# Performance work log

Hardware: AMD Instinct MI355X
Metric: run time of the kernel (lower is better)

Reference implementation:

```python
import jax, jax.numpy as jnp
import numpy as np

N = 100000          # num_nodes
E = 1600000         # num_edges
D_IN = 128          # in_channels
H = 128             # hidden_channels
D_OUT = 128         # out_channels


def setup_inputs() -> dict:
    key = jax.random.key(0)
    ks = jax.random.split(key, 12)
    s = 1.0 / np.sqrt(H)
    inp = {
        "x": jax.random.normal(ks[0], (N, D_IN), dtype=jnp.float32),
        "edge_index": jax.random.randint(ks[1], (2, E), 0, N, dtype=jnp.int64),
        "edge_weight": jax.random.uniform(ks[2], (E,), dtype=jnp.float32),
        # edge_lin (SparseLinear): weight [num_nodes, hidden], bias [hidden]
        "W_edge": jax.random.uniform(ks[3], (N, H), jnp.float32, -1.0 / np.sqrt(N), 1.0 / np.sqrt(N)),
        "b_edge": jax.random.uniform(ks[4], (H,), jnp.float32, -1.0 / np.sqrt(N), 1.0 / np.sqrt(N)),
        # node_mlp: single Linear(in_channels, hidden)
        "W_node": jax.random.uniform(ks[5], (D_IN, H), jnp.float32, -1.0 / np.sqrt(D_IN), 1.0 / np.sqrt(D_IN)),
        "b_node": jax.random.uniform(ks[6], (H,), jnp.float32, -1.0 / np.sqrt(D_IN), 1.0 / np.sqrt(D_IN)),
        # cat_lin1 / cat_lin2: Linear(hidden, hidden)
        "W_cat1": jax.random.uniform(ks[7], (H, H), jnp.float32, -s, s),
        "b_cat1": jax.random.uniform(ks[8], (H,), jnp.float32, -s, s),
        "W_cat2": jax.random.uniform(ks[9], (H, H), jnp.float32, -s, s),
        "b_cat2": jax.random.uniform(ks[10], (H,), jnp.float32, -s, s),
        # final_mlp: single Linear(hidden, out_channels)
        "W_final": jax.random.uniform(ks[11], (H, D_OUT), jnp.float32, -s, s),
        "b_final": jax.random.uniform(jax.random.fold_in(key, 99), (D_OUT,), jnp.float32, -s, s),
    }
    return inp


def reference(x, edge_index, edge_weight, W_edge, b_edge, W_node, b_node,
              W_cat1, b_cat1, W_cat2, b_cat2, W_final, b_final):
    num_nodes = W_edge.shape[0]
    src, dst = edge_index[0], edge_index[1]
    # SparseLinear: out[i] = sum_{(j,i)} edge_weight * W_edge[j]  (SpMM A @ W)
    msg = edge_weight[:, None] * W_edge[src]                      # [E, H]
    out = jax.ops.segment_sum(msg, dst, num_segments=num_nodes)  # [N, H]
    out = out + b_edge
    # out = out + cat_lin1(out)
    out = out + out @ W_cat1 + b_cat1
    # x branch: node_mlp (single linear), then residual adds
    xh = x @ W_node + b_node                                      # [N, H]
    out = out + xh
    out = out + xh @ W_cat2 + b_cat2
    # final_mlp(relu(out)): single linear
    return jax.nn.relu(out) @ W_final + b_final
```

## Files before the change

### kernel.cpp

```cpp
#include <hip/hip_runtime.h>
#include <hip/hip_fp16.h>

#define NN 100000
#define NE 1600000
#define H  128
#define CAP 48

typedef short short8 __attribute__((ext_vector_type(8)));
typedef float f32x4 __attribute__((ext_vector_type(4)));

__device__ __forceinline__ unsigned short f2bf(float f) {
    unsigned int u = __float_as_uint(f);
    u = (u + 0x7fffu + ((u >> 16) & 1u)) >> 16;
    return (unsigned short)u;
}
__device__ __forceinline__ unsigned int packbf(float a, float b) {
    return (unsigned int)f2bf(a) | ((unsigned int)f2bf(b) << 16);
}
__device__ __forceinline__ unsigned char f2e5m2(float f) {
    unsigned short h = __half_as_ushort(__float2half_rn(f));
    h = (unsigned short)(h + 0x7F + ((h >> 8) & 1));
    return (unsigned char)(h >> 8);
}
__device__ __forceinline__ float e5m2lo(unsigned int u) {
    return __half2float(__ushort_as_half((unsigned short)((u << 8) & 0xFF00)));
}
__device__ __forceinline__ float e5m2hi(unsigned int u) {
    return __half2float(__ushort_as_half((unsigned short)(u & 0xFF00)));
}
__device__ __forceinline__ float entw(unsigned int e) {
    return __half2float(__ushort_as_half((unsigned short)((e & 0x7FFFu) << 1)));
}

__global__ void fill_kernel(const int* __restrict__ ei, const float* __restrict__ ew,
                            int* __restrict__ deg, unsigned int* __restrict__ bkt) {
    int e = blockIdx.x * 256 + threadIdx.x;
    if (e >= NE) return;
    int d = ei[NE + e];
    int pos = atomicAdd(&deg[d], 1);
    if (pos < CAP) {
        unsigned short h = __half_as_ushort(__float2half_rn(ew[e]));
        bkt[d * CAP + pos] = ((unsigned int)ei[e] << 15) | (h >> 1);
    }
}

__global__ __launch_bounds__(128) void prep_weights(const float* __restrict__ W_node,
                                                    const float* __restrict__ W_cat1,
                                                    const float* __restrict__ W_cat2,
                                                    const float* __restrict__ W_final,
                                                    const float* __restrict__ b_edge,
                                                    const float* __restrict__ b_node,
                                                    const float* __restrict__ b_cat1,
                                                    const float* __restrict__ b_cat2,
                                                    unsigned short* __restrict__ m2_t,
                                                    unsigned short* __restrict__ w3_t,
                                                    unsigned short* __restrict__ wf_t,
                                                    float* __restrict__ b4) {
    int t = threadIdx.x;
    int n = blockIdx.x;
    if (n < H) {
        __shared__ float c2col[H];
        c2col[t] = W_cat2[t * H + n];
        __syncthreads();
        float dot = 0.f;
        #pragma unroll 8
        for (int j = 0; j < H; ++j)
            dot += W_node[t * H + j] * c2col[j];
        float w3 = W_node[t * H + n] + dot;
        m2_t[n * H + t] = f2bf(W_cat1[t * H + n] + (t == n ? 1.f : 0.f));
        w3_t[n * H + t] = f2bf(w3);
        wf_t[n * H + t] = f2bf(W_final[t * H + n]);
    } else {
        __shared__ float be[H], bn[H];
        be[t] = b_edge[t];
        bn[t] = b_node[t];
        __syncthreads();
        float acc = be[t] + bn[t] + b_cat1[t] + b_cat2[t];
        for (int j = 0; j < H; ++j)
            acc += be[j] * W_cat1[j * H + t] + bn[j] * W_cat2[j * H + t];
        b4[t] = acc;
    }
}

__global__ __launch_bounds__(256) void gemm_we2(const float* __restrict__ W_edge,
                                                const unsigned short* __restrict__ m2_t,
                                                unsigned char* __restrict__ we8,
                                                int nrows) {
    const int TR = 32;
    __shared__ unsigned int Wsb[TR][64];
    int row0 = blockIdx.x * TR;
    int tid = threadIdx.x;

    for (int i = tid; i < TR * H / 4; i += 256) {
        int fi = i * 4;
        int rr = fi >> 7, cc = fi & 127;
        float4 v = {0.f, 0.f, 0.f, 0.f};
        if (row0 + rr < nrows)
            v = *reinterpret_cast<const float4*>(&W_edge[(long long)(row0 + rr) * H + cc]);
        int sw = (rr & 7) << 2;
        Wsb[rr][(cc >> 1) ^ sw]       = packbf(v.x, v.y);
        Wsb[rr][((cc >> 1) + 1) ^ sw] = packbf(v.z, v.w);
    }
    __syncthreads();

    int wv = tid >> 6, lane = tid & 63;
    int rt = wv & 1, ctb = (tid >> 7) * 4;
    int l15 = lane & 15, lhi = lane >> 4;
    int arow = rt * 16 + l15, asw = arow & 7;

    f32x4 zero4 = {0.f, 0.f, 0.f, 0.f};
    f32x4 acc[4];
    acc[0] = zero4; acc[1] = zero4; acc[2] = zero4; acc[3] = zero4;
    const short8* wrow = reinterpret_cast<const short8*>(&Wsb[arow][0]);

    #pragma unroll
    for (int kt = 0; kt < 4; ++kt) {
        short8 afrag = wrow[(kt * 4 + lhi) ^ asw];
        #pragma unroll
        for (int j = 0; j < 4; ++j) {
            short8 bfrag = *reinterpret_cast<const short8*>(
                &m2_t[((ctb + j) * 16 + l15) * H + kt * 32 + lhi * 8]);
            acc[j] = __builtin_amdgcn_mfma_f32_16x16x32_bf16(afrag, bfrag, acc[j], 0, 0, 0);
        }
    }

    #pragma unroll
    for (int j = 0; j < 4; ++j) {
        int colg = (ctb + j) * 16 + l15;
        #pragma unroll
        for (int r = 0; r < 4; ++r) {
            int row = row0 + rt * 16 + lhi * 4 + r;
            if (row < nrows)
                we8[(long long)row * H + colg] = f2e5m2(acc[j][r]);
        }
    }
}

#define EDGE2(jv, ax, ay)                                                   \
    {                                                                       \
        unsigned int e0 = bkt[jv];                                          \
        unsigned int e1 = bkt[jv + 1];                                      \
        unsigned int u0 = we8u[(e0 >> 15) * 64 + lane];                     \
        unsigned int u1 = we8u[(e1 >> 15) * 64 + lane];                     \
        float w0 = entw(e0), w1 = entw(e1);                                 \
        ax += w0 * e5m2lo(u0) + w1 * e5m2lo(u1);                            \
        ay += w0 * e5m2hi(u0) + w1 * e5m2hi(u1);                            \
    }

#define EDGE1(jv, ax, ay)                                                   \
    {                                                                       \
        unsigned int e = bkt[jv];                                           \
        unsigned int u = we8u[(e >> 15) * 64 + lane];                       \
        float w = entw(e);                                                  \
        ax += w * e5m2lo(u);                                                \
        ay += w * e5m2hi(u);                                                \
    }

__global__ __launch_bounds__(256) void gather_fused(const int* __restrict__ deg,
                                                    const unsigned int* __restrict__ bkt,
                                                    const unsigned short* __restrict__ we8u,
                                                    const float* __restrict__ x,
                                                    const unsigned short* __restrict__ w3_t,
                                                    const float* __restrict__ b4,
                                                    const unsigned short* __restrict__ wf_t,
                                                    const float* __restrict__ bf,
                                                    float* __restrict__ out,
                                                    int nrows) {
    const int TR = 32;
    __shared__ unsigned int Xsb[TR][64];
    __shared__ float Gs[TR][132];
    int row0 = blockIdx.x * TR;
    int tid = threadIdx.x;

    for (int i = tid; i < TR * H / 4; i += 256) {
        int fi = i * 4;
        int rr = fi >> 7, cc = fi & 127;
        float4 xv = *reinterpret_cast<const float4*>(&x[(long long)(row0 + rr) * H + cc]);
        int sw = (rr & 7) << 2;
        Xsb[rr][(cc >> 1) ^ sw]       = packbf(xv.x, xv.y);
        Xsb[rr][((cc >> 1) + 1) ^ sw] = packbf(xv.z, xv.w);
    }

    int wv = tid >> 6;
    int lane = tid & 63;
    #pragma unroll
    for (int rq = 0; rq < 2; ++rq) {
        int rrA = wv * 8 + rq * 4;
        int dA = row0 + rrA;
        float axA = 0.f, ayA = 0.f, axB = 0.f, ayB = 0.f;
        float axC = 0.f, ayC = 0.f, axD = 0.f, ayD = 0.f;

        int dgA = __builtin_amdgcn_readfirstlane(deg[dA]);
        int dgB = __builtin_amdgcn_readfirstlane(deg[dA + 1]);
        int dgC = __builtin_amdgcn_readfirstlane(deg[dA + 2]);
        int dgD = __builtin_amdgcn_readfirstlane(deg[dA + 3]);
        if (dgA > CAP) dgA = CAP;
        if (dgB > CAP) dgB = CAP;
        if (dgC > CAP) dgC = CAP;
        if (dgD > CAP) dgD = CAP;
        int jA = dA * CAP,      i1A = jA + dgA;
        int jB = (dA + 1) * CAP, i1B = jB + dgB;
        int jC = (dA + 2) * CAP, i1C = jC + dgC;
        int jD = (dA + 3) * CAP, i1D = jD + dgD;

        while (jA + 2 <= i1A && jB + 2 <= i1B && jC + 2 <= i1C && jD + 2 <= i1D) {
            unsigned int eA0 = bkt[jA];
            unsigned int eA1 = bkt[jA + 1];
            unsigned int eB0 = bkt[jB];
            unsigned int eB1 = bkt[jB + 1];
            unsigned int eC0 = bkt[jC];
            unsigned int eC1 = bkt[jC + 1];
            unsigned int eD0 = bkt[jD];
            unsigned int eD1 = bkt[jD + 1];
            unsigned int uA0 = we8u[(eA0 >> 15) * 64 + lane];
            unsigned int uA1 = we8u[(eA1 >> 15) * 64 + lane];
            unsigned int uB0 = we8u[(eB0 >> 15) * 64 + lane];
            unsigned int uB1 = we8u[(eB1 >> 15) * 64 + lane];
            unsigned int uC0 = we8u[(eC0 >> 15) * 64 + lane];
            unsigned int uC1 = we8u[(eC1 >> 15) * 64 + lane];
            unsigned int uD0 = we8u[(eD0 >> 15) * 64 + lane];
            unsigned int uD1 = we8u[(eD1 >> 15) * 64 + lane];
            float wA0 = entw(eA0), wA1 = entw(eA1);
            float wB0 = entw(eB0), wB1 = entw(eB1);
            float wC0 = entw(eC0), wC1 = entw(eC1);
            float wD0 = entw(eD0), wD1 = entw(eD1);
            axA += wA0 * e5m2lo(uA0) + wA1 * e5m2lo(uA1);
            ayA += wA0 * e5m2hi(uA0) + wA1 * e5m2hi(uA1);
            axB += wB0 * e5m2lo(uB0) + wB1 * e5m2lo(uB1);
            ayB += wB0 * e5m2hi(uB0) + wB1 * e5m2hi(uB1);
            axC += wC0 * e5m2lo(uC0) + wC1 * e5m2lo(uC1);
            ayC += wC0 * e5m2hi(uC0) + wC1 * e5m2hi(uC1);
            axD += wD0 * e5m2lo(uD0) + wD1 * e5m2lo(uD1);
            ayD += wD0 * e5m2hi(uD0) + wD1 * e5m2hi(uD1);
            jA += 2; jB += 2; jC += 2; jD += 2;
        }
        while (jA + 2 <= i1A && jB + 2 <= i1B) {
            EDGE2(jA, axA, ayA)
            EDGE2(jB, axB, ayB)
            jA += 2; jB += 2;
        }
        for (; jA + 2 <= i1A; jA += 2) EDGE2(jA, axA, ayA)
        if (jA < i1A) EDGE1(jA, axA, ayA)
        for (; jB + 2 <= i1B; jB += 2) EDGE2(jB, axB, ayB)
        if (jB < i1B) EDGE1(jB, axB, ayB)
        while (jC + 2 <= i1C && jD + 2 <= i1D) {
            EDGE2(jC, axC, ayC)
            EDGE2(jD, axD, ayD)
            jC += 2; jD += 2;
        }
        for (; jC + 2 <= i1C; jC += 2) EDGE2(jC, axC, ayC)
        if (jC < i1C) EDGE1(jC, axC, ayC)
        for (; jD + 2 <= i1D; jD += 2) EDGE2(jD, axD, ayD)
        if (jD < i1D) EDGE1(jD, axD, ayD)

        *reinterpret_cast<float2*>(&Gs[rrA][2 * lane])     = make_float2(axA, ayA);
        *reinterpret_cast<float2*>(&Gs[rrA + 1][2 * lane]) = make_float2(axB, ayB);
        *reinterpret_cast<float2*>(&Gs[rrA + 2][2 * lane]) = make_float2(axC, ayC);
        *reinterpret_cast<float2*>(&Gs[rrA + 3][2 * lane]) = make_float2(axD, ayD);
    }
    __syncthreads();

    int rt = wv & 1, ctb = (tid >> 7) * 4;
    int l15 = lane & 15, lhi = lane >> 4;
    int arow = rt * 16 + l15, asw = arow & 7;

    f32x4 acc[4];
    #pragma unroll
    for (int j = 0; j < 4; ++j) {
        int colg = (ctb + j) * 16 + l15;
        float bv = b4[colg];
        #pragma unroll
        for (int r = 0; r < 4; ++r)
            acc[j][r] = Gs[rt * 16 + lhi * 4 + r][colg] + bv;
    }
    __syncthreads();

    const short8* xsrow = reinterpret_cast<const short8*>(&Xsb[arow][0]);
    #pragma unroll
    for (int kt = 0; kt < 4; ++kt) {
        short8 afrag = xsrow[(kt * 4 + lhi) ^ asw];
        #pragma unroll
        for (int j = 0; j < 4; ++j) {
            short8 bfrag = *reinterpret_cast<const short8*>(
                &w3_t[((ctb + j) * 16 + l15) * H + kt * 32 + lhi * 8]);
            acc[j] = __builtin_amdgcn_mfma_f32_16x16x32_bf16(afrag, bfrag, acc[j], 0, 0, 0);
        }
    }

    unsigned short* t4s = reinterpret_cast<unsigned short*>(Gs);
    #pragma unroll
    for (int j = 0; j < 4; ++j) {
        int colg = (ctb + j) * 16 + l15;
        #pragma unroll
        for (int r = 0; r < 4; ++r) {
            int row = rt * 16 + lhi * 4 + r;
            float v = fmaxf(acc[j][r], 0.f);
            t4s[row * 128 + (colg ^ ((row & 7) << 3))] = f2bf(v);
        }
    }
    __syncthreads();

    f32x4 zero4 = {0.f, 0.f, 0.f, 0.f};
    f32x4 acc2[4];
    acc2[0] = zero4; acc2[1] = zero4; acc2[2] = zero4; acc2[3] = zero4;
    const short8* t4row = reinterpret_cast<const short8*>(t4s + arow * 128);

    #pragma unroll
    for (int kt = 0; kt < 4; ++kt) {
        short8 afrag = t4row[(kt * 4 + lhi) ^ asw];
        #pragma unroll
        for (int j = 0; j < 4; ++j) {
            short8 bfrag = *reinterpret_cast<const short8*>(
                &wf_t[((ctb + j) * 16 + l15) * H + kt * 32 + lhi * 8]);
            acc2[j] = __builtin_amdgcn_mfma_f32_16x16x32_bf16(afrag, bfrag, acc2[j], 0, 0, 0);
        }
    }

    #pragma unroll
    for (int j = 0; j < 4; ++j) {
        int colg = (ctb + j) * 16 + l15;
        float bv = bf[colg];
        #pragma unroll
        for (int r = 0; r < 4; ++r) {
            int row = row0 + rt * 16 + lhi * 4 + r;
            out[(long long)row * H + colg] = acc2[j][r] + bv;
        }
    }
}

extern "C" void kernel_launch(void* const* d_in, const int* in_sizes, int n_in,
                              void* d_out, int out_size, void* d_ws, size_t ws_size,
                              hipStream_t stream) {
    const float* x       = (const float*)d_in[0];
    const int*   ei      = (const int*)d_in[1];
    const float* ew      = (const float*)d_in[2];
    const float* W_edge  = (const float*)d_in[3];
    const float* b_edge  = (const float*)d_in[4];
    const float* W_node  = (const float*)d_in[5];
    const float* b_node  = (const float*)d_in[6];
    const float* W_cat1  = (const float*)d_in[7];
    const float* b_cat1  = (const float*)d_in[8];
    const float* W_cat2  = (const float*)d_in[9];
    const float* b_cat2  = (const float*)d_in[10];
    const float* W_final = (const float*)d_in[11];
    const float* b_final = (const float*)d_in[12];
    float* out = (float*)d_out;

    int* deg = (int*)d_ws;
    unsigned int* bkt = (unsigned int*)(deg + NN);
    unsigned char* we8 = (unsigned char*)(bkt + (size_t)NN * CAP);
    unsigned short* m2_t = (unsigned short*)(we8 + (size_t)NN * H);
    unsigned short* w3_t = m2_t + H * H;
    unsigned short* wf_t = w3_t + H * H;
    float* b4 = (float*)(wf_t + H * H);

    hipMemsetAsync(deg, 0, NN * sizeof(int), stream);
    fill_kernel<<<(NE + 255) / 256, 256, 0, stream>>>(ei, ew, deg, bkt);

    prep_weights<<<H + 1, H, 0, stream>>>(W_node, W_cat1, W_cat2, W_final,
                                          b_edge, b_node, b_cat1, b_cat2,
                                          m2_t, w3_t, wf_t, b4);
    gemm_we2<<<(NN + 31) / 32, 256, 0, stream>>>(W_edge, m2_t, we8, NN);

    gather_fused<<<(NN + 31) / 32, 256, 0, stream>>>(deg, bkt, (const unsigned short*)we8,
                                                     x, w3_t, b4, wf_t, b_final, out, NN);
}
```

Measured before the change: 305.7 us.

## Interleave eight destination rows per wave and fold degree zeroing into prep kernel

The gather loop now walks all eight of a wave's destination rows together, so each iteration issues sixteen independent bucket and W_edge row loads instead of eight, raising memory-level parallelism for the random gathers. The separate hipMemsetAsync of the degree array is replaced by extra blocks in prep_weights, removing one launch and moving prep_weights ahead of fill_kernel. The cost is more live registers in gather_fused, which may lower occupancy, and the eight-way loop exits as soon as the shortest of the eight rows runs out, leaving more work to the pairwise tail loops.

```diff
diff --git a/kernel.cpp b/kernel.cpp
--- a/kernel.cpp
+++ b/kernel.cpp
@@ -55,7 +55,8 @@
                                                     unsigned short* __restrict__ m2_t,
                                                     unsigned short* __restrict__ w3_t,
                                                     unsigned short* __restrict__ wf_t,
-                                                    float* __restrict__ b4) {
+                                                    float* __restrict__ b4,
+                                                    int* __restrict__ deg) {
     int t = threadIdx.x;
     int n = blockIdx.x;
     if (n < H) {
@@ -70,7 +71,7 @@
         m2_t[n * H + t] = f2bf(W_cat1[t * H + n] + (t == n ? 1.f : 0.f));
         w3_t[n * H + t] = f2bf(w3);
         wf_t[n * H + t] = f2bf(W_final[t * H + n]);
-    } else {
+    } else if (n == H) {
         __shared__ float be[H], bn[H];
         be[t] = b_edge[t];
         bn[t] = b_node[t];
@@ -79,6 +80,9 @@
         for (int j = 0; j < H; ++j)
             acc += be[j] * W_cat1[j * H + t] + bn[j] * W_cat2[j * H + t];
         b4[t] = acc;
+    } else {
+        int i = (n - H - 1) * 128 + t;
+        if (i < NN) deg[i] = 0;
     }
 }
 
@@ -154,6 +158,14 @@
         float w = entw(e);                                                  \
         ax += w * e5m2lo(u);                                                \
         ay += w * e5m2hi(u);                                                \
+    }
+
+#define STEP8(eN0, eN1, uN0, uN1, jv, ax, ay)                               \
+    {                                                                       \
+        float w0 = entw(eN0), w1 = entw(eN1);                               \
+        ax += w0 * e5m2lo(uN0) + w1 * e5m2lo(uN1);                          \
+        ay += w0 * e5m2hi(uN0) + w1 * e5m2hi(uN1);                          \
+        jv += 2;                                                            \
     }
 
 __global__ __launch_bounds__(256) void gather_fused(const int* __restrict__ deg,
@@ -183,35 +195,48 @@
 
     int wv = tid >> 6;
     int lane = tid & 63;
-    #pragma unroll
-    for (int rq = 0; rq < 2; ++rq) {
-        int rrA = wv * 8 + rq * 4;
-        int dA = row0 + rrA;
+    {
+        int base = row0 + wv * 8;
         float axA = 0.f, ayA = 0.f, axB = 0.f, ayB = 0.f;
         float axC = 0.f, ayC = 0.f, axD = 0.f, ayD = 0.f;
-
-        int dgA = __builtin_amdgcn_readfirstlane(deg[dA]);
-        int dgB = __builtin_amdgcn_readfirstlane(deg[dA + 1]);
-        int dgC = __builtin_amdgcn_readfirstlane(deg[dA + 2]);
-        int dgD = __builtin_amdgcn_readfirstlane(deg[dA + 3]);
+        float axE = 0.f, ayE = 0.f, axF = 0.f, ayF = 0.f;
+        float axG = 0.f, ayG = 0.f, axH = 0.f, ayH = 0.f;
+
+        int dgA = __builtin_amdgcn_readfirstlane(deg[base]);
+        int dgB = __builtin_amdgcn_readfirstlane(deg[base + 1]);
+        int dgC = __builtin_amdgcn_readfirstlane(deg[base + 2]);
+        int dgD = __builtin_amdgcn_readfirstlane(deg[base + 3]);
+        int dgE = __builtin_amdgcn_readfirstlane(deg[base + 4]);
+        int dgF = __builtin_amdgcn_readfirstlane(deg[base + 5]);
+        int dgG = __builtin_amdgcn_readfirstlane(deg[base + 6]);
+        int dgH = __builtin_amdgcn_readfirstlane(deg[base + 7]);
         if (dgA > CAP) dgA = CAP;
         if (dgB > CAP) dgB = CAP;
         if (dgC > CAP) dgC = CAP;
         if (dgD > CAP) dgD = CAP;
-        int jA = dA * CAP,      i1A = jA + dgA;
-        int jB = (dA + 1) * CAP, i1B = jB + dgB;
-        int jC = (dA + 2) * CAP, i1C = jC + dgC;
-        int jD = (dA + 3) * CAP, i1D = jD + dgD;
-
-        while (jA + 2 <= i1A && jB + 2 <= i1B && jC + 2 <= i1C && jD + 2 <= i1D) {
-            unsigned int eA0 = bkt[jA];
-            unsigned int eA1 = bkt[jA + 1];
-            unsigned int eB0 = bkt[jB];
-            unsigned int eB1 = bkt[jB + 1];
-            unsigned int eC0 = bkt[jC];
-            unsigned int eC1 = bkt[jC + 1];
-            unsigned int eD0 = bkt[jD];
-            unsigned int eD1 = bkt[jD + 1];
+        if (dgE > CAP) dgE = CAP;
+        if (dgF > CAP) dgF = CAP;
+        if (dgG > CAP) dgG = CAP;
+        if (dgH > CAP) dgH = CAP;
+        int jA = base * CAP,        i1A = jA + dgA;
+        int jB = (base + 1) * CAP,  i1B = jB + dgB;
+        int jC = (base + 2) * CAP,  i1C = jC + dgC;
+        int jD = (base + 3) * CAP,  i1D = jD + dgD;
+        int jE = (base + 4) * CAP,  i1E = jE + dgE;
+        int jF = (base + 5) * CAP,  i1F = jF + dgF;
+        int jG = (base + 6) * CAP,  i1G = jG + dgG;
+        int jH = (base + 7) * CAP,  i1H = jH + dgH;
+
+        while (jA + 2 <= i1A && jB + 2 <= i1B && jC + 2 <= i1C && jD + 2 <= i1D &&
+               jE + 2 <= i1E && jF + 2 <= i1F && jG + 2 <= i1G && jH + 2 <= i1H) {
+            unsigned int eA0 = bkt[jA], eA1 = bkt[jA + 1];
+            unsigned int eB0 = bkt[jB], eB1 = bkt[jB + 1];
+            unsigned int eC0 = bkt[jC], eC1 = bkt[jC + 1];
+            unsigned int eD0 = bkt[jD], eD1 = bkt[jD + 1];
+            unsigned int eE0 = bkt[jE], eE1 = bkt[jE + 1];
+            unsigned int eF0 = bkt[jF], eF1 = bkt[jF + 1];
+            unsigned int eG0 = bkt[jG], eG1 = bkt[jG + 1];
+            unsigned int eH0 = bkt[jH], eH1 = bkt[jH + 1];
             unsigned int uA0 = we8u[(eA0 >> 15) * 64 + lane];
             unsigned int uA1 = we8u[(eA1 >> 15) * 64 + lane];
             unsigned int uB0 = we8u[(eB0 >> 15) * 64 + lane];
@@ -220,43 +245,53 @@
             unsigned int uC1 = we8u[(eC1 >> 15) * 64 + lane];
             unsigned int uD0 = we8u[(eD0 >> 15) * 64 + lane];
             unsigned int uD1 = we8u[(eD1 >> 15) * 64 + lane];
-            float wA0 = entw(eA0), wA1 = entw(eA1);
-            float wB0 = entw(eB0), wB1 = entw(eB1);
-            float wC0 = entw(eC0), wC1 = entw(eC1);
-            float wD0 = entw(eD0), wD1 = entw(eD1);
-            axA += wA0 * e5m2lo(uA0) + wA1 * e5m2lo(uA1);
-            ayA += wA0 * e5m2hi(uA0) + wA1 * e5m2hi(uA1);
-            axB += wB0 * e5m2lo(uB0) + wB1 * e5m2lo(uB1);
-            ayB += wB0 * e5m2hi(uB0) + wB1 * e5m2hi(uB1);
-            axC += wC0 * e5m2lo(uC0) + wC1 * e5m2lo(uC1);
-            ayC += wC0 * e5m2hi(uC0) + wC1 * e5m2hi(uC1);
-            axD += wD0 * e5m2lo(uD0) + wD1 * e5m2lo(uD1);
-            ayD += wD0 * e5m2hi(uD0) + wD1 * e5m2hi(uD1);
-            jA += 2; jB += 2; jC += 2; jD += 2;
-        }
-        while (jA + 2 <= i1A && jB + 2 <= i1B) {
-            EDGE2(jA, axA, ayA)
-            EDGE2(jB, axB, ayB)
-            jA += 2; jB += 2;
-        }
+            unsigned int uE0 = we8u[(eE0 >> 15) * 64 + lane];
+            unsigned int uE1 = we8u[(eE1 >> 15) * 64 + lane];
+            unsigned int uF0 = we8u[(eF0 >> 15) * 64 + lane];
+            unsigned int uF1 = we8u[(eF1 >> 15) * 64 + lane];
+            unsigned int uG0 = we8u[(eG0 >> 15) * 64 + lane];
+            unsigned int uG1 = we8u[(eG1 >> 15) * 64 + lane];
+            unsigned int uH0 = we8u[(eH0 >> 15) * 64 + lane];
+            unsigned int uH1 = we8u[(eH1 >> 15) * 64 + lane];
+            STEP8(eA0, eA1, uA0, uA1, jA, axA, ayA)
+            STEP8(eB0, eB1, uB0, uB1, jB, axB, ayB)
+            STEP8(eC0, eC1, uC0, uC1, jC, axC, ayC)
+            STEP8(eD0, eD1, uD0, uD1, jD, axD, ayD)
+            STEP8(eE0, eE1, uE0, uE1, jE, axE, ayE)
+            STEP8(eF0, eF1, uF0, uF1, jF, axF, ayF)
+            STEP8(eG0, eG1, uG0, uG1, jG, axG, ayG)
+            STEP8(eH0, eH1, uH0, uH1, jH, axH, ayH)
+        }
+        while (jA + 2 <= i1A && jB + 2 <= i1B) { EDGE2(jA, axA, ayA) EDGE2(jB, axB, ayB) jA += 2; jB += 2; }
         for (; jA + 2 <= i1A; jA += 2) EDGE2(jA, axA, ayA)
         if (jA < i1A) EDGE1(jA, axA, ayA)
         for (; jB + 2 <= i1B; jB += 2) EDGE2(jB, axB, ayB)
         if (jB < i1B) EDGE1(jB, axB, ayB)
-        while (jC + 2 <= i1C && jD + 2 <= i1D) {
-            EDGE2(jC, axC, ayC)
-            EDGE2(jD, axD, ayD)
-            jC += 2; jD += 2;
-        }
+        while (jC + 2 <= i1C && jD + 2 <= i1D) { EDGE2(jC, axC, ayC) EDGE2(jD, axD, ayD) jC += 2; jD += 2; }
         for (; jC + 2 <= i1C; jC += 2) EDGE2(jC, axC, ayC)
         if (jC < i1C) EDGE1(jC, axC, ayC)
         for (; jD + 2 <= i1D; jD += 2) EDGE2(jD, axD, ayD)
         if (jD < i1D) EDGE1(jD, axD, ayD)
-
-        *reinterpret_cast<float2*>(&Gs[rrA][2 * lane])     = make_float2(axA, ayA);
-        *reinterpret_cast<float2*>(&Gs[rrA + 1][2 * lane]) = make_float2(axB, ayB);
-        *reinterpret_cast<float2*>(&Gs[rrA + 2][2 * lane]) = make_float2(axC, ayC);
-        *reinterpret_cast<float2*>(&Gs[rrA + 3][2 * lane]) = make_float2(axD, ayD);
+        while (jE + 2 <= i1E && jF + 2 <= i1F) { EDGE2(jE, axE, ayE) EDGE2(jF, axF, ayF) jE += 2; jF += 2; }
+        for (; jE + 2 <= i1E; jE += 2) EDGE2(jE, axE, ayE)
+        if (jE < i1E) EDGE1(jE, axE, ayE)
+        for (; jF + 2 <= i1F; jF += 2) EDGE2(jF, axF, ayF)
+        if (jF < i1F) EDGE1(jF, axF, ayF)
+        while (jG + 2 <= i1G && jH + 2 <= i1H) { EDGE2(jG, axG, ayG) EDGE2(jH, axH, ayH) jG += 2; jH += 2; }
+        for (; jG + 2 <= i1G; jG += 2) EDGE2(jG, axG, ayG)
+        if (jG < i1G) EDGE1(jG, axG, ayG)
+        for (; jH + 2 <= i1H; jH += 2) EDGE2(jH, axH, ayH)
+        if (jH < i1H) EDGE1(jH, axH, ayH)
+
+        int rr = wv * 8;
+        *reinterpret_cast<float2*>(&Gs[rr][2 * lane])     = make_float2(axA, ayA);
+        *reinterpret_cast<float2*>(&Gs[rr + 1][2 * lane]) = make_float2(axB, ayB);
+        *reinterpret_cast<float2*>(&Gs[rr + 2][2 * lane]) = make_float2(axC, ayC);
+        *reinterpret_cast<float2*>(&Gs[rr + 3][2 * lane]) = make_float2(axD, ayD);
+        *reinterpret_cast<float2*>(&Gs[rr + 4][2 * lane]) = make_float2(axE, ayE);
+        *reinterpret_cast<float2*>(&Gs[rr + 5][2 * lane]) = make_float2(axF, ayF);
+        *reinterpret_cast<float2*>(&Gs[rr + 6][2 * lane]) = make_float2(axG, ayG);
+        *reinterpret_cast<float2*>(&Gs[rr + 7][2 * lane]) = make_float2(axH, ayH);
     }
     __syncthreads();
 
@@ -354,12 +389,12 @@
     unsigned short* wf_t = w3_t + H * H;
     float* b4 = (float*)(wf_t + H * H);
 
-    hipMemsetAsync(deg, 0, NN * sizeof(int), stream);
+    int zero_blocks = (NN + 127) / 128;
+    prep_weights<<<H + 1 + zero_blocks, H, 0, stream>>>(W_node, W_cat1, W_cat2, W_final,
+                                                        b_edge, b_node, b_cat1, b_cat2,
+                                                        m2_t, w3_t, wf_t, b4, deg);
     fill_kernel<<<(NE + 255) / 256, 256, 0, stream>>>(ei, ew, deg, bkt);
 
-    prep_weights<<<H + 1, H, 0, stream>>>(W_node, W_cat1, W_cat2, W_final,
-                                          b_edge, b_node, b_cat1, b_cat2,
-                                          m2_t, w3_t, wf_t, b4);
     gemm_we2<<<(NN + 31) / 32, 256, 0, stream>>>(W_edge, m2_t, we8, NN);
 
     gather_fused<<<(NN + 31) / 32, 256, 0, stream>>>(deg, bkt, (const unsigned short*)we8,
```

New measurement: 297.2 us. 1.03x faster.
